# Kernel tuning notes

Hardware: AMD Instinct MI355X
Metric: run time of the kernel (lower is better)

## Reference

```python
import jax, jax.numpy as jnp
import numpy as np

B, S, D = 8, 2048, 512

def setup_inputs() -> dict:
    key = jax.random.key(0)
    ks = jax.random.split(key, 4)
    scale = 1.0 / np.sqrt(D)
    x = jax.random.normal(ks[0], (B, S, D), dtype=jnp.float32)
    Wq = jax.random.normal(ks[1], (D, D), dtype=jnp.float32) * scale
    Wk = jax.random.normal(ks[2], (D, D), dtype=jnp.float32) * scale
    Wv = jax.random.normal(ks[3], (D, D), dtype=jnp.float32) * scale
    bq = jnp.zeros((D,), jnp.float32)
    bk = jnp.zeros((D,), jnp.float32)
    bv = jnp.zeros((D,), jnp.float32)
    return {"x": x, "Wq": Wq, "bq": bq, "Wk": Wk, "bk": bk, "Wv": Wv, "bv": bv}

def reference(x, Wq, bq, Wk, bk, Wv, bv):
    # Q, K, V projections: [B,S,D]
    Q = jnp.einsum('bsd,de->bse', x, Wq) + bq
    K = jnp.einsum('bsd,de->bse', x, Wk) + bk
    V = jnp.einsum('bsd,de->bse', x, Wv) + bv
    scale = jnp.sqrt(jnp.asarray(Q.shape[-1], Q.dtype))
    scores = jnp.einsum('bqd,bkd->bqk', Q, K) / scale  # [B,S,S]
    attn = jax.nn.softmax(scores, axis=-1)
    context = jnp.einsum('bqk,bkd->bqd', attn, V)  # [B,S,D]
    return context
```

## Files before the change

### kernel.cpp

```cpp
#include <hip/hip_runtime.h>
#include <hip/hip_bf16.h>

#define B_ 8
#define S_ 2048
#define D_ 512

typedef __attribute__((ext_vector_type(8))) short short8;
typedef __attribute__((ext_vector_type(4))) float f32x4;

static __device__ __forceinline__ unsigned short f2bf(float f) {
    union { float f; unsigned u; } v; v.f = f;
    unsigned r = v.u + 0x7FFFu + ((v.u >> 16) & 1u);
    return (unsigned short)(r >> 16);
}

static __device__ __forceinline__ float fexp2(float x) {
    float r; asm("v_exp_f32 %0, %1" : "=v"(r) : "v"(x)); return r;
}

static __device__ __forceinline__ void gl_lds16(const void* g, void* l) {
    __builtin_amdgcn_global_load_lds(
        (const __attribute__((address_space(1))) unsigned int*)g,
        (__attribute__((address_space(3))) unsigned int*)l, 16, 0, 0);
}

__global__ void k_prep(const float* __restrict__ x,
                       const float* __restrict__ Wq, const float* __restrict__ Wk,
                       const float* __restrict__ Wv,
                       unsigned short* __restrict__ xb, unsigned short* __restrict__ Wt,
                       float* __restrict__ l) {
    int bid = blockIdx.x;
    if (bid < 4096) {
        int i = bid * 256 + threadIdx.x;
        const float4* p = (const float4*)x + (size_t)i * 2;
        float4 a = p[0], b = p[1];
        union { unsigned short u[8]; uint4 v; } o;
        o.u[0] = f2bf(a.x); o.u[1] = f2bf(a.y); o.u[2] = f2bf(a.z); o.u[3] = f2bf(a.w);
        o.u[4] = f2bf(b.x); o.u[5] = f2bf(b.y); o.u[6] = f2bf(b.z); o.u[7] = f2bf(b.w);
        ((uint4*)xb)[i] = o.v;
    } else if (bid < 7168) {
        int idx = (bid - 4096) * 256 + threadIdx.x;
        int z = idx >> 18;
        int r = idx & 262143;
        int e = r >> 9, d = r & 511;
        const float* W = (z == 0) ? Wq : ((z == 1) ? Wk : Wv);
        Wt[idx] = f2bf(W[d * 512 + e]);
    } else {
        l[(bid - 7168) * 256 + threadIdx.x] = 0.f;
    }
}

__global__ __launch_bounds__(256, 4) void k_qkv(
    const unsigned short* __restrict__ xb, const unsigned short* __restrict__ Wt,
    const float* __restrict__ biasq, const float* __restrict__ biask,
    const float* __restrict__ biasv,
    unsigned short* __restrict__ Qb, unsigned short* __restrict__ Kb,
    unsigned short* __restrict__ Vs) {
  __shared__ __align__(16) unsigned char smA[16384];
  __shared__ __align__(16) unsigned char smB[16384];
  const int z = blockIdx.z;
  const unsigned short* W = Wt + (size_t)z * (D_ * D_);
  const int lane = threadIdx.x & 63, wid = threadIdx.x >> 6;
  const int c = lane & 15, g = lane >> 4;
  const int wr = wid >> 1, wc = wid & 1;
  const int m_blk = blockIdx.x * 128;
  const int n_blk = blockIdx.y * 128;

  const int src_sw = ((lane & 7) * 16) ^ (((lane >> 3) & 7) << 4);
  const unsigned char* ga = (const unsigned char*)xb
      + (size_t)(m_blk + wid * 32 + (lane >> 3)) * 1024;
  const unsigned char* gb = (const unsigned char*)W
      + (size_t)(n_blk + wid * 32 + (lane >> 3)) * 1024;
  unsigned char* la = smA + wid * 4096;
  unsigned char* lb = smB + wid * 4096;

  f32x4 acc[4][4];
#pragma unroll
  for (int mi = 0; mi < 4; ++mi)
#pragma unroll
    for (int ni = 0; ni < 4; ++ni) acc[mi][ni] = (f32x4){0.f, 0.f, 0.f, 0.f};

  for (int step = 0; step < 8; ++step) {
    __syncthreads();
#pragma unroll
    for (int i = 0; i < 4; ++i) {
      gl_lds16(ga + (size_t)i * 8192 + step * 128 + src_sw, la + i * 1024);
      gl_lds16(gb + (size_t)i * 8192 + step * 128 + src_sw, lb + i * 1024);
    }
    __syncthreads();
#pragma unroll
    for (int kc = 0; kc < 2; ++kc) {
      const int ro = (kc * 64 + g * 16) ^ ((c & 7) << 4);
      short8 af[4], bf[4];
#pragma unroll
      for (int mi = 0; mi < 4; ++mi)
        af[mi] = *(const short8*)(smA + (wr * 64 + mi * 16 + c) * 128 + ro);
#pragma unroll
      for (int ni = 0; ni < 4; ++ni)
        bf[ni] = *(const short8*)(smB + (wc * 64 + ni * 16 + c) * 128 + ro);
#pragma unroll
      for (int mi = 0; mi < 4; ++mi)
#pragma unroll
        for (int ni = 0; ni < 4; ++ni)
          acc[mi][ni] = __builtin_amdgcn_mfma_f32_16x16x32_bf16(af[mi], bf[ni], acc[mi][ni], 0, 0, 0);
    }
  }

  const int m0 = m_blk + wr * 64;
  const int n0 = n_blk + wc * 64;
  if (z < 2) {
    const float* bias = (z == 0) ? biasq : biask;
    unsigned short* outp = (z == 0) ? Qb : Kb;
    const float scl = (z == 0) ? 0.0637587238f : 1.0f;
#pragma unroll
    for (int ni = 0; ni < 4; ++ni) {
      int cc = n0 + ni * 16 + c;
      float bb = bias[cc];
#pragma unroll
      for (int mi = 0; mi < 4; ++mi)
#pragma unroll
        for (int r = 0; r < 4; ++r) {
          int row = m0 + mi * 16 + g * 4 + r;
          outp[(size_t)row * D_ + cc] = f2bf((acc[mi][ni][r] + bb) * scl);
        }
    }
  } else {
#pragma unroll
    for (int ni = 0; ni < 4; ++ni) {
      int e = n0 + ni * 16 + c;
      float bb = biasv[e];
#pragma unroll
      for (int mi = 0; mi < 4; ++mi) {
        int row = m0 + mi * 16 + g * 4;
        int bi = row >> 11, sl = row & 2047;
        int t = sl >> 5, kvin = sl & 31;
        union { unsigned short u[4]; uint2 v; } pk;
#pragma unroll
        for (int r = 0; r < 4; ++r) pk.u[r] = f2bf(acc[mi][ni][r] + bb);
        *(uint2*)(Vs + ((((size_t)bi * 64 + t) * 512) + e) * 32 + kvin) = pk.v;
      }
    }
  }
}

__global__ __launch_bounds__(256, 4) void k_pa(
    const unsigned short* __restrict__ Qb, const unsigned short* __restrict__ Kb,
    unsigned short* __restrict__ P, float* __restrict__ l,
    int b_base, int bc) {
  __shared__ __align__(16) unsigned char smA[16384];
  __shared__ __align__(16) unsigned char smB[16384];
  const int lane = threadIdx.x & 63, wid = threadIdx.x >> 6;
  const int c = lane & 15, g = lane >> 4;
  const int wr = wid >> 1, wc = wid & 1;
  const int bloc = blockIdx.x % bc;
  const int tile = blockIdx.x / bc;
  const int b = b_base + bloc;
  const int m_blk = (tile & 15) * 128;
  const int n_blk = (tile >> 4) * 128;
  unsigned short* Pb = P + (size_t)bloc * S_ * S_;

  const int src_sw = ((lane & 7) * 16) ^ (((lane >> 3) & 7) << 4);
  const unsigned char* ga = (const unsigned char*)(Kb + (size_t)b * S_ * D_)
      + (size_t)(m_blk + wid * 32 + (lane >> 3)) * 1024;
  const unsigned char* gb = (const unsigned char*)(Qb + (size_t)b * S_ * D_)
      + (size_t)(n_blk + wid * 32 + (lane >> 3)) * 1024;
  unsigned char* la = smA + wid * 4096;
  unsigned char* lb = smB + wid * 4096;

  f32x4 acc[4][4];
#pragma unroll
  for (int mi = 0; mi < 4; ++mi)
#pragma unroll
    for (int ni = 0; ni < 4; ++ni) acc[mi][ni] = (f32x4){0.f, 0.f, 0.f, 0.f};

  for (int step = 0; step < 8; ++step) {
    __syncthreads();
#pragma unroll
    for (int i = 0; i < 4; ++i) {
      gl_lds16(ga + (size_t)i * 8192 + step * 128 + src_sw, la + i * 1024);
      gl_lds16(gb + (size_t)i * 8192 + step * 128 + src_sw, lb + i * 1024);
    }
    __syncthreads();
#pragma unroll
    for (int kc = 0; kc < 2; ++kc) {
      const int ro = (kc * 64 + g * 16) ^ ((c & 7) << 4);
      short8 af[4], bf[4];
#pragma unroll
      for (int mi = 0; mi < 4; ++mi)
        af[mi] = *(const short8*)(smA + (wr * 64 + mi * 16 + c) * 128 + ro);
#pragma unroll
      for (int ni = 0; ni < 4; ++ni)
        bf[ni] = *(const short8*)(smB + (wc * 64 + ni * 16 + c) * 128 + ro);
#pragma unroll
      for (int mi = 0; mi < 4; ++mi)
#pragma unroll
        for (int ni = 0; ni < 4; ++ni)
          acc[mi][ni] = __builtin_amdgcn_mfma_f32_16x16x32_bf16(af[mi], bf[ni], acc[mi][ni], 0, 0, 0);
    }
  }

  const float SH = 11.5415603f;
  float psum[4] = {0.f, 0.f, 0.f, 0.f};
  __syncthreads();
#pragma unroll
  for (int ni = 0; ni < 4; ++ni) {
    const int q_loc = wc * 64 + ni * 16 + c;
#pragma unroll
    for (int mi = 0; mi < 4; ++mi) {
      float p0 = fexp2(acc[mi][ni][0] - SH);
      float p1 = fexp2(acc[mi][ni][1] - SH);
      float p2 = fexp2(acc[mi][ni][2] - SH);
      float p3 = fexp2(acc[mi][ni][3] - SH);
      psum[ni] += (p0 + p1) + (p2 + p3);
      unsigned w0, w1;
      asm("v_cvt_pk_bf16_f32 %0, %1, %2" : "=v"(w0) : "v"(p0), "v"(p1));
      asm("v_cvt_pk_bf16_f32 %0, %1, %2" : "=v"(w1) : "v"(p2), "v"(p3));
      const int kv2 = (wr * 64 + mi * 16 + g * 4) * 2;
      *(uint2*)(smA + q_loc * 256 + (kv2 ^ ((q_loc & 15) << 4))) = (uint2){w0, w1};
    }
  }
#pragma unroll
  for (int ni = 0; ni < 4; ++ni) {
    float v = psum[ni];
    v += __shfl_xor(v, 16);
    v += __shfl_xor(v, 32);
    if (g == 0)
      atomicAdd(l + b * S_ + n_blk + wc * 64 + ni * 16 + c, v);
  }
  __syncthreads();
#pragma unroll
  for (int i = 0; i < 8; ++i) {
    const int q_loc = wid * 32 + i * 4 + (lane >> 4);
    const int kvb = (lane & 15) * 16;
    uint4 v = *(const uint4*)(smA + q_loc * 256 + (kvb ^ ((q_loc & 15) << 4)));
    *(uint4*)((unsigned char*)Pb + (size_t)(n_blk + q_loc) * 4096 + m_blk * 2 + kvb) = v;
  }
}

__global__ __launch_bounds__(256, 4) void k_pb(
    const unsigned short* __restrict__ P, const unsigned short* __restrict__ Vs,
    const float* __restrict__ l, float* __restrict__ out,
    int b_base, int bc) {
  __shared__ __align__(16) unsigned char smA[16384];
  __shared__ __align__(16) unsigned char smB[8192];
  const int lane = threadIdx.x & 63, wid = threadIdx.x >> 6;
  const int c = lane & 15, g = lane >> 4;
  const int wr = wid >> 1, wc = wid & 1;
  const int bloc = blockIdx.x % bc;
  const int tile = blockIdx.x / bc;
  const int b = b_base + bloc;
  const int m_blk = (tile & 3) * 128;
  const int n_blk = (tile >> 2) * 64;
  const unsigned short* Pb = P + (size_t)bloc * S_ * S_;
  const unsigned char* Vsb = (const unsigned char*)(Vs + (size_t)b * 64 * 512 * 32);

  const int src_sw = ((lane & 7) * 16) ^ (((lane >> 3) & 7) << 4);
  const unsigned char* ga = Vsb + (size_t)(src_sw >> 6) * 32768
      + (size_t)(m_blk + wid * 32 + (lane >> 3)) * 64 + (src_sw & 63);
  const unsigned char* gb = (const unsigned char*)Pb
      + (size_t)(n_blk + wid * 16 + (lane >> 3)) * 4096;
  unsigned char* la = smA + wid * 4096;
  unsigned char* lb = smB + wid * 2048;

  f32x4 acc[4][2];
#pragma unroll
  for (int mi = 0; mi < 4; ++mi)
#pragma unroll
    for (int ni = 0; ni < 2; ++ni) acc[mi][ni] = (f32x4){0.f, 0.f, 0.f, 0.f};

  for (int step = 0; step < 32; ++step) {
    __syncthreads();
#pragma unroll
    for (int i = 0; i < 4; ++i)
      gl_lds16(ga + (size_t)step * 65536 + i * 512, la + i * 1024);
#pragma unroll
    for (int i = 0; i < 2; ++i)
      gl_lds16(gb + (size_t)i * 32768 + step * 128 + src_sw, lb + i * 1024);
    __syncthreads();
#pragma unroll
    for (int kc = 0; kc < 2; ++kc) {
      const int ro = (kc * 64 + g * 16) ^ ((c & 7) << 4);
      short8 af[4], bf[2];
#pragma unroll
      for (int mi = 0; mi < 4; ++mi)
        af[mi] = *(const short8*)(smA + (wr * 64 + mi * 16 + c) * 128 + ro);
#pragma unroll
      for (int ni = 0; ni < 2; ++ni)
        bf[ni] = *(const short8*)(smB + (wc * 32 + ni * 16 + c) * 128 + ro);
#pragma unroll
      for (int mi = 0; mi < 4; ++mi)
#pragma unroll
        for (int ni = 0; ni < 2; ++ni)
          acc[mi][ni] = __builtin_amdgcn_mfma_f32_16x16x32_bf16(af[mi], bf[ni], acc[mi][ni], 0, 0, 0);
    }
  }

  const int m0 = m_blk + wr * 64;
  const int n0 = n_blk + wc * 32;
  float* ob = out + (size_t)b * S_ * D_;
#pragma unroll
  for (int ni = 0; ni < 2; ++ni) {
    const int q = n0 + ni * 16 + c;
    const float inv = 1.f / l[b * S_ + q];
#pragma unroll
    for (int mi = 0; mi < 4; ++mi) {
      float4 v;
      v.x = acc[mi][ni][0] * inv; v.y = acc[mi][ni][1] * inv;
      v.z = acc[mi][ni][2] * inv; v.w = acc[mi][ni][3] * inv;
      *(float4*)(ob + (size_t)q * D_ + m0 + mi * 16 + g * 4) = v;
    }
  }
}

extern "C" void kernel_launch(void* const* d_in, const int* in_sizes, int n_in,
                              void* d_out, int out_size, void* d_ws, size_t ws_size,
                              hipStream_t stream) {
  const float* x  = (const float*)d_in[0];
  const float* Wq = (const float*)d_in[1];
  const float* bq = (const float*)d_in[2];
  const float* Wk = (const float*)d_in[3];
  const float* bk = (const float*)d_in[4];
  const float* Wv = (const float*)d_in[5];
  const float* bv = (const float*)d_in[6];
  float* out = (float*)d_out;

  unsigned short* xb = (unsigned short*)d_ws;
  unsigned short* Wt = xb + (size_t)16384 * 512;
  unsigned short* Qb = Wt + (size_t)3 * 512 * 512;
  unsigned short* Kb = Qb + (size_t)16384 * 512;
  unsigned short* Vs = Kb + (size_t)16384 * 512;
  float* l = (float*)(Vs + (size_t)8 * 64 * 512 * 32);
  unsigned short* Pfull = (unsigned short*)(l + 8 * 2048);
  const size_t full_need =
      (size_t)((unsigned char*)(Pfull + (size_t)8 * 2048 * 2048) - (unsigned char*)d_ws);

  k_prep<<<dim3(7232), dim3(256), 0, stream>>>(x, Wq, Wk, Wv, xb, Wt, l);
  k_qkv<<<dim3(128, 4, 3), dim3(256), 0, stream>>>(xb, Wt, bq, bk, bv, Qb, Kb, Vs);

  if (ws_size >= full_need) {
    k_pa<<<dim3(2048), dim3(256), 0, stream>>>(Qb, Kb, Pfull, l, 0, 8);
    k_pb<<<dim3(1024), dim3(256), 0, stream>>>(Pfull, Vs, l, out, 0, 8);
  } else {
    unsigned short* P2 = xb;
    for (int g2 = 0; g2 < 4; ++g2) {
      k_pa<<<dim3(512), dim3(256), 0, stream>>>(Qb, Kb, P2, l, g2 * 2, 2);
      k_pb<<<dim3(256), dim3(256), 0, stream>>>(P2, Vs, l, out, g2 * 2, 2);
    }
  }
}
```

Baseline: 125.9 us.

## Enlarge PV kernel tiles to 256x128 with double-buffered LDS prefetch

Rewrites the P·V kernel to use 512-thread blocks computing 256x128 output tiles, with LDS double-buffering so the next K-step's V and P tiles are loaded asynchronously while the current step's MFMAs run. It also raises wave priority around the MFMA bursts and needs one barrier per step instead of two. The larger tiles cut redundant reads of P and V. In exchange it uses 96KB of LDS per block and only 256 blocks (64 in the fallback path), which lowers occupancy and may underfill the GPU's compute units.

Result: faster. 122.1 us (-3.1%).

```diff
diff --git a/kernel.cpp b/kernel.cpp
--- a/kernel.cpp
+++ b/kernel.cpp
@@ -237,77 +237,123 @@
   }
 }
 
-__global__ __launch_bounds__(256, 4) void k_pb(
+__global__ __launch_bounds__(512, 1) void k_pb(
     const unsigned short* __restrict__ P, const unsigned short* __restrict__ Vs,
     const float* __restrict__ l, float* __restrict__ out,
     int b_base, int bc) {
-  __shared__ __align__(16) unsigned char smA[16384];
-  __shared__ __align__(16) unsigned char smB[8192];
+  __shared__ __align__(16) unsigned char sm[98304];
   const int lane = threadIdx.x & 63, wid = threadIdx.x >> 6;
   const int c = lane & 15, g = lane >> 4;
-  const int wr = wid >> 1, wc = wid & 1;
+  const int wm = wid >> 2, wn = wid & 3;
   const int bloc = blockIdx.x % bc;
   const int tile = blockIdx.x / bc;
   const int b = b_base + bloc;
-  const int m_blk = (tile & 3) * 128;
-  const int n_blk = (tile >> 2) * 64;
-  const unsigned short* Pb = P + (size_t)bloc * S_ * S_;
+  const int m_blk = (tile & 1) * 256;
+  const int n_blk = (tile >> 1) * 128;
+  const unsigned char* Pb = (const unsigned char*)(P + (size_t)bloc * S_ * S_);
   const unsigned char* Vsb = (const unsigned char*)(Vs + (size_t)b * 64 * 512 * 32);
 
   const int src_sw = ((lane & 7) * 16) ^ (((lane >> 3) & 7) << 4);
-  const unsigned char* ga = Vsb + (size_t)(src_sw >> 6) * 32768
-      + (size_t)(m_blk + wid * 32 + (lane >> 3)) * 64 + (src_sw & 63);
-  const unsigned char* gb = (const unsigned char*)Pb
-      + (size_t)(n_blk + wid * 16 + (lane >> 3)) * 4096;
-  unsigned char* la = smA + wid * 4096;
-  unsigned char* lb = smB + wid * 2048;
-
-  f32x4 acc[4][2];
-#pragma unroll
-  for (int mi = 0; mi < 4; ++mi)
-#pragma unroll
-    for (int ni = 0; ni < 2; ++ni) acc[mi][ni] = (f32x4){0.f, 0.f, 0.f, 0.f};
-
-  for (int step = 0; step < 32; ++step) {
-    __syncthreads();
-#pragma unroll
-    for (int i = 0; i < 4; ++i)
-      gl_lds16(ga + (size_t)step * 65536 + i * 512, la + i * 1024);
-#pragma unroll
-    for (int i = 0; i < 2; ++i)
-      gl_lds16(gb + (size_t)i * 32768 + step * 128 + src_sw, lb + i * 1024);
-    __syncthreads();
-#pragma unroll
-    for (int kc = 0; kc < 2; ++kc) {
-      const int ro = (kc * 64 + g * 16) ^ ((c & 7) << 4);
-      short8 af[4], bf[2];
-#pragma unroll
-      for (int mi = 0; mi < 4; ++mi)
-        af[mi] = *(const short8*)(smA + (wr * 64 + mi * 16 + c) * 128 + ro);
-#pragma unroll
-      for (int ni = 0; ni < 2; ++ni)
-        bf[ni] = *(const short8*)(smB + (wc * 32 + ni * 16 + c) * 128 + ro);
-#pragma unroll
-      for (int mi = 0; mi < 4; ++mi)
-#pragma unroll
-        for (int ni = 0; ni < 2; ++ni)
-          acc[mi][ni] = __builtin_amdgcn_mfma_f32_16x16x32_bf16(af[mi], bf[ni], acc[mi][ni], 0, 0, 0);
-    }
-  }
-
-  const int m0 = m_blk + wr * 64;
-  const int n0 = n_blk + wc * 32;
+  const unsigned char* gA0 = Vsb + (size_t)(src_sw >> 6) * 32768
+      + (size_t)(m_blk + (lane >> 3)) * 64 + (src_sw & 63);
+  const unsigned char* gB0 = Pb + (size_t)(n_blk + (lane >> 3)) * 4096 + src_sw;
+
+#define STG_A(h_, t_, bp_)                                                   \
+  {                                                                          \
+    _Pragma("unroll")                                                        \
+    for (int i = 0; i < 2; ++i) {                                            \
+      int rl = wid * 16 + i * 8;                                             \
+      int pbv = (rl & 63) + ((rl & 64) << 1) + (h_) * 64;                    \
+      gl_lds16(gA0 + (size_t)(t_) * 65536 + (size_t)pbv * 64,                \
+               sm + (bp_) * 32768 + pbv * 128);                              \
+    }                                                                        \
+  }
+#define STG_B(h_, t_, bp_)                                                   \
+  {                                                                          \
+    int rl = wid * 8;                                                        \
+    int pbv = (rl & 8) + (h_) * 16 + ((rl >> 4) << 5);                       \
+    gl_lds16(gB0 + (size_t)pbv * 4096 + (t_) * 128,                          \
+             sm + 65536 + (bp_) * 16384 + pbv * 128);                        \
+  }
+
+  f32x4 acc[8][2];
+#pragma unroll
+  for (int a = 0; a < 8; ++a)
+#pragma unroll
+    for (int ni = 0; ni < 2; ++ni) acc[a][ni] = (f32x4){0.f, 0.f, 0.f, 0.f};
+
+  STG_A(0, 0, 0); STG_B(0, 0, 0); STG_A(1, 0, 0); STG_B(1, 0, 0);
+  __syncthreads();
+
+  for (int t = 0; t < 32; ++t) {
+    const int cb = t & 1, nb = cb ^ 1;
+    const unsigned char* Ab = sm + cb * 32768;
+    const unsigned char* Bb = sm + 65536 + cb * 16384;
+    short8 bfr[2][2];
+#pragma unroll
+    for (int ni = 0; ni < 2; ++ni) {
+      int row = wn * 32 + ni * 16 + c;
+#pragma unroll
+      for (int kc = 0; kc < 2; ++kc)
+        bfr[ni][kc] = *(const short8*)(Bb + row * 128 + ((kc * 64 + g * 16) ^ ((c & 7) << 4)));
+    }
+    {
+      short8 af[4][2];
+#pragma unroll
+      for (int mi = 0; mi < 4; ++mi) {
+        int row = wm * 128 + mi * 16 + c;
+#pragma unroll
+        for (int kc = 0; kc < 2; ++kc)
+          af[mi][kc] = *(const short8*)(Ab + row * 128 + ((kc * 64 + g * 16) ^ ((c & 7) << 4)));
+      }
+      if (t < 31) { STG_A(0, t + 1, nb); STG_B(0, t + 1, nb); }
+      __builtin_amdgcn_s_setprio(1);
+#pragma unroll
+      for (int kc = 0; kc < 2; ++kc)
+#pragma unroll
+        for (int mi = 0; mi < 4; ++mi)
+#pragma unroll
+          for (int ni = 0; ni < 2; ++ni)
+            acc[mi][ni] = __builtin_amdgcn_mfma_f32_16x16x32_bf16(af[mi][kc], bfr[ni][kc], acc[mi][ni], 0, 0, 0);
+      __builtin_amdgcn_s_setprio(0);
+    }
+    {
+      short8 af[4][2];
+#pragma unroll
+      for (int mi = 0; mi < 4; ++mi) {
+        int row = wm * 128 + 64 + mi * 16 + c;
+#pragma unroll
+        for (int kc = 0; kc < 2; ++kc)
+          af[mi][kc] = *(const short8*)(Ab + row * 128 + ((kc * 64 + g * 16) ^ ((c & 7) << 4)));
+      }
+      if (t < 31) { STG_A(1, t + 1, nb); STG_B(1, t + 1, nb); }
+      __builtin_amdgcn_s_setprio(1);
+#pragma unroll
+      for (int kc = 0; kc < 2; ++kc)
+#pragma unroll
+        for (int mi = 0; mi < 4; ++mi)
+#pragma unroll
+          for (int ni = 0; ni < 2; ++ni)
+            acc[4 + mi][ni] = __builtin_amdgcn_mfma_f32_16x16x32_bf16(af[mi][kc], bfr[ni][kc], acc[4 + mi][ni], 0, 0, 0);
+      __builtin_amdgcn_s_setprio(0);
+    }
+    __syncthreads();
+  }
+#undef STG_A
+#undef STG_B
+
   float* ob = out + (size_t)b * S_ * D_;
 #pragma unroll
   for (int ni = 0; ni < 2; ++ni) {
-    const int q = n0 + ni * 16 + c;
+    const int q = n_blk + wn * 32 + ni * 16 + c;
     const float inv = 1.f / l[b * S_ + q];
 #pragma unroll
-    for (int mi = 0; mi < 4; ++mi) {
+    for (int a = 0; a < 8; ++a) {
+      const int d0 = m_blk + wm * 128 + (a >> 2) * 64 + (a & 3) * 16 + g * 4;
       float4 v;
-      v.x = acc[mi][ni][0] * inv; v.y = acc[mi][ni][1] * inv;
-      v.z = acc[mi][ni][2] * inv; v.w = acc[mi][ni][3] * inv;
-      *(float4*)(ob + (size_t)q * D_ + m0 + mi * 16 + g * 4) = v;
+      v.x = acc[a][ni][0] * inv; v.y = acc[a][ni][1] * inv;
+      v.z = acc[a][ni][2] * inv; v.w = acc[a][ni][3] * inv;
+      *(float4*)(ob + (size_t)q * D_ + d0) = v;
     }
   }
 }
@@ -339,12 +385,12 @@
 
   if (ws_size >= full_need) {
     k_pa<<<dim3(2048), dim3(256), 0, stream>>>(Qb, Kb, Pfull, l, 0, 8);
-    k_pb<<<dim3(1024), dim3(256), 0, stream>>>(Pfull, Vs, l, out, 0, 8);
+    k_pb<<<dim3(256),  dim3(512), 0, stream>>>(Pfull, Vs, l, out, 0, 8);
   } else {
     unsigned short* P2 = xb;
     for (int g2 = 0; g2 < 4; ++g2) {
       k_pa<<<dim3(512), dim3(256), 0, stream>>>(Qb, Kb, P2, l, g2 * 2, 2);
-      k_pb<<<dim3(256), dim3(256), 0, stream>>>(P2, Vs, l, out, g2 * 2, 2);
-    }
-  }
-}
+      k_pb<<<dim3(64), dim3(512), 0, stream>>>(P2, Vs, l, out, g2 * 2, 2);
+    }
+  }
+}
```
